# Optimization experiments

Hardware: AMD Instinct MI355X
Metric: run time of the kernel (lower is better)

## Reference

```python
import jax, jax.numpy as jnp
import numpy as np


def setup_inputs() -> dict:
    key = jax.random.key(0)
    ks = jax.random.split(key, 6)
    B, S, H, I, E = 2, 1024, 1024, 2816, 8
    W = 0.02  # weight init scale
    return {
        "x": jax.random.normal(ks[0], (B, S, H), jnp.float32),
        "w_router": jax.random.normal(ks[1], (H, E), jnp.float32) * W,
        "w_gate": jax.random.normal(ks[2], (E, H, I), jnp.float32) * W,
        "w_up": jax.random.normal(ks[3], (E, H, I), jnp.float32) * W,
        "w_down": jax.random.normal(ks[4], (E, I, H), jnp.float32) * W,
        "b_down": jnp.zeros((E, H), jnp.float32),
    }


def reference(x, w_router, w_gate, w_up, w_down, b_down):
    # Eval path of PrunedLlamaSMoEBlock: noiseless router, top-k select, softmax
    # over selected logits, SwiGLU experts, scatter-add combine.
    NUM_SELECTS = 2
    T = x.shape[0] * x.shape[1]
    E = w_router.shape[1]
    flat_x = x.reshape(T, -1)                      # [T,H]

    logits = flat_x @ w_router                     # [T,E]
    top_vals, top_idx = jax.lax.top_k(logits, NUM_SELECTS)   # [T,k]
    gw = jax.nn.softmax(top_vals.astype(jnp.float32), axis=1).astype(x.dtype)

    # Dense combine weights: combine[t,e] = sum_k gw[t,k] * (top_idx[t,k]==e)
    combine = jnp.zeros((T, E), x.dtype).at[
        jnp.arange(T)[:, None], top_idx
    ].add(gw)                                      # [T,E]

    # SwiGLU experts over all tokens (weighted by combine, zero if unselected)
    g = jnp.einsum("th,ehi->tei", flat_x, w_gate)  # [T,E,I]
    u = jnp.einsum("th,ehi->tei", flat_x, w_up)    # [T,E,I]
    a = jax.nn.silu(g) * u                         # [T,E,I]
    y = jnp.einsum("tei,eih->teh", a, w_down) + b_down[None]  # [T,E,H]

    out = jnp.einsum("te,teh->th", combine, y)     # [T,H]
    return out.reshape(x.shape)
```

## Files before the change

### kernel.cpp

```cpp
#include <hip/hip_runtime.h>
#include <math.h>

#define HD __device__ __forceinline__

constexpr int TT = 2048;
constexpr int HH = 1024;
constexpr int II = 2816;
constexpr int EE = 8;
constexpr int NK1 = HH / 64;
constexpr int NK2 = II / 64;
constexpr int KS2 = 2;
constexpr int HALF2 = NK2 / KS2;
constexpr int MAXTILES = 40;
constexpr int NSLOT = 2 * TT;

typedef short  bf16x8  __attribute__((ext_vector_type(8)));
typedef float  floatx4 __attribute__((ext_vector_type(4)));
typedef unsigned short ushortx8 __attribute__((ext_vector_type(8)));

constexpr size_t OFF_XB    = 0;
constexpr size_t OFF_WGT   = OFF_XB    + (size_t)TT*HH*2;
constexpr size_t OFF_WUT   = OFF_WGT   + (size_t)EE*II*HH*2;
constexpr size_t OFF_WDT   = OFF_WUT   + (size_t)EE*II*HH*2;
constexpr size_t OFF_ABUF  = OFF_WDT   + (size_t)EE*HH*II*2;
constexpr size_t OFF_CNT   = OFF_ABUF  + (size_t)2*TT*II*2;
constexpr size_t OFF_OFFS  = OFF_CNT   + 256;
constexpr size_t OFF_MDESC = OFF_OFFS  + 256;
constexpr size_t OFF_EMETA = OFF_MDESC + 256;
constexpr size_t OFF_WMETA = OFF_EMETA + 16384;
constexpr size_t OFF_TLIST = OFF_WMETA + 16384;
constexpr size_t OFF_SLOT  = OFF_TLIST + 16384;
constexpr size_t OFF_YBUF  = OFF_WGT;

HD unsigned short f2bf(float f) {
  union { float f; unsigned int u; } v; v.f = f;
  return (unsigned short)((v.u + 0x7fffu + ((v.u >> 16) & 1u)) >> 16);
}

HD void load_lds16(const void* gptr, void* lptr) {
  __builtin_amdgcn_global_load_lds(
      (const __attribute__((address_space(1))) void*)gptr,
      (__attribute__((address_space(3))) void*)lptr,
      16, 0, 0);
}

__global__ __launch_bounds__(256)
void prep_kernel(const float* __restrict__ x, unsigned short* __restrict__ xb,
                 int* __restrict__ counts) {
  const int i = blockIdx.x * blockDim.x + threadIdx.x;
  if (i < EE) counts[i] = 0;
  float4 v = ((const float4*)x)[i];
  ushort4 o;
  o.x = f2bf(v.x); o.y = f2bf(v.y); o.z = f2bf(v.z); o.w = f2bf(v.w);
  ((ushort4*)xb)[i] = o;
}

__global__ __launch_bounds__(256)
void transpose_cast_kernel(const float* __restrict__ wg, const float* __restrict__ wu,
                           const float* __restrict__ wd,
                           unsigned short* __restrict__ wgt, unsigned short* __restrict__ wut,
                           unsigned short* __restrict__ wdt) {
  const int e = blockIdx.y / 3;
  const int t = blockIdx.y % 3;
  const float* src; unsigned short* dst; int R, C;
  if (t == 0)      { src = wg; dst = wgt; R = HH; C = II; }
  else if (t == 1) { src = wu; dst = wut; R = HH; C = II; }
  else             { src = wd; dst = wdt; R = II; C = HH; }
  const int nct = C / 128;
  const int rt = blockIdx.x / nct;
  const int ct = blockIdx.x % nct;
  const size_t base = (size_t)e * R * C;
  const int R0 = rt * 64;
  const int C0 = ct * 128;

  const int lane = threadIdx.x & 63;
  const int wave = threadIdx.x >> 6;
  const int r0 = R0 + (lane & 7) * 8;
  const int c0 = C0 + wave * 32 + (lane >> 3) * 4;

  floatx4 v[8];
  const float* sp = src + base + (size_t)r0 * C + c0;
#pragma unroll
  for (int j = 0; j < 8; ++j)
    v[j] = __builtin_nontemporal_load((const floatx4*)(sp + (size_t)j * C));

  unsigned short* dp = dst + base + (size_t)c0 * R + r0;
#pragma unroll
  for (int jj = 0; jj < 4; ++jj) {
    ushortx8 o;
#pragma unroll
    for (int j = 0; j < 8; ++j) o[j] = f2bf(v[j][jj]);
    *(ushortx8*)(dp + (size_t)jj * R) = o;
  }
}

__global__ __launch_bounds__(64)
void router_kernel(const float* __restrict__ x, const float* __restrict__ w_router,
                   int* __restrict__ counts, int* __restrict__ emeta, float* __restrict__ wmeta) {
  const int t = blockIdx.x;
  const int lane = threadIdx.x;
  float acc[EE];
#pragma unroll
  for (int e = 0; e < EE; ++e) acc[e] = 0.f;
  for (int h = lane; h < HH; h += 64) {
    const float xv = x[(size_t)t * HH + h];
    const float* wr = w_router + (size_t)h * EE;
#pragma unroll
    for (int e = 0; e < EE; ++e) acc[e] += xv * wr[e];
  }
#pragma unroll
  for (int e = 0; e < EE; ++e) {
#pragma unroll
    for (int off = 32; off > 0; off >>= 1) acc[e] += __shfl_xor(acc[e], off, 64);
  }
  if (lane == 0) {
    int e0 = 0; float v0 = acc[0];
#pragma unroll
    for (int e = 1; e < EE; ++e) if (acc[e] > v0) { v0 = acc[e]; e0 = e; }
    int e1 = -1; float v1 = -3.4e38f;
#pragma unroll
    for (int e = 0; e < EE; ++e) if (e != e0 && acc[e] > v1) { v1 = acc[e]; e1 = e; }
    const float ex = __expf(v1 - v0);
    const float s  = 1.f + ex;
    emeta[2 * t] = e0; emeta[2 * t + 1] = e1;
    wmeta[2 * t] = 1.f / s; wmeta[2 * t + 1] = ex / s;
    atomicAdd(&counts[e0], 1);
    atomicAdd(&counts[e1], 1);
  }
}

__global__ __launch_bounds__(256)
void scanfill_kernel(const int* __restrict__ counts, const int* __restrict__ emeta,
                     int* __restrict__ offsets, int* __restrict__ mdesc,
                     int* __restrict__ token_list, int* __restrict__ slotmap) {
  const int e = blockIdx.x;
  const int tid = threadIdx.x;
  int off_e = 0;
#pragma unroll
  for (int i = 0; i < EE; ++i) { const int c = counts[i]; if (i < e) off_e += c; }
  if (e == 0 && tid == 0) {
    int s = 0, nt = 0;
    for (int i = 0; i < EE; ++i) {
      const int c = counts[i];
      offsets[i] = s;
      for (int m = 0; m < c; m += 128) mdesc[1 + nt++] = (i << 20) | m;
      s += c;
    }
    offsets[EE] = s;
    mdesc[0] = nt;
  }
  constexpr int CH = TT / 256;
  const int t0 = tid * CH;
  int cnt = 0;
  for (int k = 0; k < CH; ++k) {
    const int t = t0 + k;
    if (emeta[2 * t] == e) ++cnt;
    if (emeta[2 * t + 1] == e) ++cnt;
  }
  __shared__ int s_scan[256];
  s_scan[tid] = cnt;
  __syncthreads();
  int v = cnt;
  for (int d = 1; d < 256; d <<= 1) {
    const int add = (tid >= d) ? s_scan[tid - d] : 0;
    __syncthreads();
    v += add;
    s_scan[tid] = v;
    __syncthreads();
  }
  int pos = off_e + (v - cnt);
  for (int k = 0; k < CH; ++k) {
    const int t = t0 + k;
#pragma unroll
    for (int s = 0; s < 2; ++s) {
      if (emeta[2 * t + s] == e) {
        token_list[pos] = t;
        slotmap[2 * t + s] = pos;
        ++pos;
      }
    }
  }
}

__global__ __launch_bounds__(256, 4)
void gemm1_kernel(const unsigned short* __restrict__ xb,
                  const unsigned short* __restrict__ wgt,
                  const unsigned short* __restrict__ wut,
                  const int* __restrict__ offsets,
                  const int* __restrict__ mdesc,
                  const int* __restrict__ token_list,
                  unsigned short* __restrict__ Abuf) {
  if ((int)blockIdx.y >= mdesc[0]) return;
  const int d = mdesc[1 + blockIdx.y];
  const int e = d >> 20;
  const int m_base = d & 0xFFFFF;
  const int off_e = offsets[e];
  const int n_e = offsets[e + 1] - off_e;
  const int n_base = blockIdx.x * 64;

  __shared__ __attribute__((aligned(16))) unsigned short ldsA[128 * 64];
  __shared__ __attribute__((aligned(16))) unsigned short ldsG[64 * 64];
  __shared__ __attribute__((aligned(16))) unsigned short ldsU[64 * 64];

  const int tid = threadIdx.x;
  const int wave = tid >> 6;
  const int lane = tid & 63;
  const int quad = lane >> 4;
  const int l16 = lane & 15;
  const int wave_m = (wave & 1) * 64;
  const int wave_n = (wave >> 1) * 32;

  const int srow = lane >> 3;
  const int clog = (lane & 7) ^ srow;

  const unsigned short* gA[4];
  const unsigned short* gG[2];
  const unsigned short* gU[2];
#pragma unroll
  for (int it = 0; it < 4; ++it) {
    const int r = it * 32 + wave * 8 + srow;
    int ar = m_base + r; if (ar > n_e - 1) ar = n_e - 1;
    const int tok = token_list[off_e + ar];
    gA[it] = xb + (size_t)tok * HH + clog * 8;
  }
#pragma unroll
  for (int it = 0; it < 2; ++it) {
    const int r = it * 32 + wave * 8 + srow;
    gG[it] = wgt + ((size_t)e * II + (n_base + r)) * HH + clog * 8;
    gU[it] = wut + ((size_t)e * II + (n_base + r)) * HH + clog * 8;
  }

  floatx4 accG[4][2], accU[4][2];
  const floatx4 fz = {0.f, 0.f, 0.f, 0.f};
#pragma unroll
  for (int i = 0; i < 4; ++i)
#pragma unroll
    for (int j = 0; j < 2; ++j) { accG[i][j] = fz; accU[i][j] = fz; }

  for (int kt = 0; kt < NK1; ++kt) {
    const int k0 = kt * 64;
#pragma unroll
    for (int it = 0; it < 4; ++it)
      load_lds16(gA[it] + k0, &ldsA[(it * 32 + wave * 8) * 64]);
#pragma unroll
    for (int it = 0; it < 2; ++it) {
      load_lds16(gG[it] + k0, &ldsG[(it * 32 + wave * 8) * 64]);
      load_lds16(gU[it] + k0, &ldsU[(it * 32 + wave * 8) * 64]);
    }
    __syncthreads();
#pragma unroll
    for (int ks = 0; ks < 2; ++ks) {
      bf16x8 af[4], bg[2], bu[2];
#pragma unroll
      for (int f = 0; f < 4; ++f) {
        const int rowA = wave_m + f * 16 + l16;
        const int cA = (ks * 4 + quad) ^ (rowA & 7);
        af[f] = *(const bf16x8*)&ldsA[rowA * 64 + cA * 8];
      }
#pragma unroll
      for (int f = 0; f < 2; ++f) {
        const int rowB = wave_n + f * 16 + l16;
        const int cB = (ks * 4 + quad) ^ (rowB & 7);
        bg[f] = *(const bf16x8*)&ldsG[rowB * 64 + cB * 8];
        bu[f] = *(const bf16x8*)&ldsU[rowB * 64 + cB * 8];
      }
#pragma unroll
      for (int mf = 0; mf < 4; ++mf)
#pragma unroll
        for (int nf = 0; nf < 2; ++nf) {
          accG[mf][nf] = __builtin_amdgcn_mfma_f32_16x16x32_bf16(af[mf], bg[nf], accG[mf][nf], 0, 0, 0);
          accU[mf][nf] = __builtin_amdgcn_mfma_f32_16x16x32_bf16(af[mf], bu[nf], accU[mf][nf], 0, 0, 0);
        }
    }
    __syncthreads();
  }

#pragma unroll
  for (int mf = 0; mf < 4; ++mf)
#pragma unroll
    for (int nf = 0; nf < 2; ++nf) {
      const int col = n_base + wave_n + nf * 16 + l16;
#pragma unroll
      for (int j = 0; j < 4; ++j) {
        const int r = m_base + wave_m + mf * 16 + quad * 4 + j;
        if (r < n_e) {
          const float g = accG[mf][nf][j];
          const float u = accU[mf][nf][j];
          const float a = (g / (1.f + __expf(-g))) * u;
          Abuf[(size_t)(off_e + r) * II + col] = f2bf(a);
        }
      }
    }
}

__global__ __launch_bounds__(256, 3)
void gemm2_kernel(const unsigned short* __restrict__ Abuf,
                  const unsigned short* __restrict__ wdt,
                  const int* __restrict__ offsets,
                  const int* __restrict__ mdesc,
                  float* __restrict__ Ybuf) {
  if ((int)blockIdx.y >= mdesc[0]) return;
  const int d = mdesc[1 + blockIdx.y];
  const int e = d >> 20;
  const int m_base = d & 0xFFFFF;
  const int off_e = offsets[e];
  const int n_e = offsets[e + 1] - off_e;
  const int n_base = blockIdx.x * 128;
  const int split = blockIdx.z;
  const int kt_lo = split * HALF2;
  const int kt_hi = kt_lo + HALF2;

  __shared__ __attribute__((aligned(16))) unsigned short ldsA[128 * 64];
  __shared__ __attribute__((aligned(16))) unsigned short ldsB[128 * 64];

  const int tid = threadIdx.x;
  const int wave = tid >> 6;
  const int lane = tid & 63;
  const int quad = lane >> 4;
  const int l16 = lane & 15;
  const int wave_m = (wave & 1) * 64;
  const int wave_n = (wave >> 1) * 64;

  const int srow = lane >> 3;
  const int clog = (lane & 7) ^ srow;

  const unsigned short* gA[4];
  const unsigned short* gB[4];
#pragma unroll
  for (int it = 0; it < 4; ++it) {
    const int r = it * 32 + wave * 8 + srow;
    int ar = m_base + r; if (ar > n_e - 1) ar = n_e - 1;
    gA[it] = Abuf + (size_t)(off_e + ar) * II + clog * 8;
  }
#pragma unroll
  for (int it = 0; it < 4; ++it) {
    const int r = it * 32 + wave * 8 + srow;
    gB[it] = wdt + ((size_t)e * HH + (n_base + r)) * II + clog * 8;
  }

  floatx4 acc[4][4];
  const floatx4 fz = {0.f, 0.f, 0.f, 0.f};
#pragma unroll
  for (int i = 0; i < 4; ++i)
#pragma unroll
    for (int j = 0; j < 4; ++j) acc[i][j] = fz;

  for (int kt = kt_lo; kt < kt_hi; ++kt) {
    const int k0 = kt * 64;
#pragma unroll
    for (int it = 0; it < 4; ++it)
      load_lds16(gA[it] + k0, &ldsA[(it * 32 + wave * 8) * 64]);
#pragma unroll
    for (int it = 0; it < 4; ++it)
      load_lds16(gB[it] + k0, &ldsB[(it * 32 + wave * 8) * 64]);
    __syncthreads();
#pragma unroll
    for (int ks = 0; ks < 2; ++ks) {
      bf16x8 af[4], bf[4];
#pragma unroll
      for (int f = 0; f < 4; ++f) {
        const int rowA = wave_m + f * 16 + l16;
        const int cA = (ks * 4 + quad) ^ (rowA & 7);
        af[f] = *(const bf16x8*)&ldsA[rowA * 64 + cA * 8];
      }
#pragma unroll
      for (int f = 0; f < 4; ++f) {
        const int rowB = wave_n + f * 16 + l16;
        const int cB = (ks * 4 + quad) ^ (rowB & 7);
        bf[f] = *(const bf16x8*)&ldsB[rowB * 64 + cB * 8];
      }
#pragma unroll
      for (int mf = 0; mf < 4; ++mf)
#pragma unroll
        for (int nf = 0; nf < 4; ++nf)
          acc[mf][nf] = __builtin_amdgcn_mfma_f32_16x16x32_bf16(af[mf], bf[nf], acc[mf][nf], 0, 0, 0);
    }
    __syncthreads();
  }

  float* yb = Ybuf + (size_t)split * NSLOT * HH;
#pragma unroll
  for (int mf = 0; mf < 4; ++mf)
#pragma unroll
    for (int nf = 0; nf < 4; ++nf) {
      const int col = n_base + wave_n + nf * 16 + l16;
#pragma unroll
      for (int j = 0; j < 4; ++j) {
        const int r = m_base + wave_m + mf * 16 + quad * 4 + j;
        if (r < n_e)
          yb[(size_t)(off_e + r) * HH + col] = acc[mf][nf][j];
      }
    }
}

__global__ __launch_bounds__(256)
void combine_kernel(const float* __restrict__ Ybuf, const int* __restrict__ slotmap,
                    const int* __restrict__ emeta, const float* __restrict__ wmeta,
                    const float* __restrict__ b_down, float* __restrict__ out) {
  const int t = blockIdx.x;
  const int c = threadIdx.x;
  const int s0 = slotmap[2 * t], s1 = slotmap[2 * t + 1];
  const int e0 = emeta[2 * t], e1 = emeta[2 * t + 1];
  const float g0 = wmeta[2 * t], g1 = wmeta[2 * t + 1];
  const float4 y00 = ((const float4*)(Ybuf + (size_t)s0 * HH))[c];
  const float4 y01 = ((const float4*)(Ybuf + ((size_t)NSLOT + s0) * HH))[c];
  const float4 y10 = ((const float4*)(Ybuf + (size_t)s1 * HH))[c];
  const float4 y11 = ((const float4*)(Ybuf + ((size_t)NSLOT + s1) * HH))[c];
  const float4 b0 = ((const float4*)(b_down + (size_t)e0 * HH))[c];
  const float4 b1 = ((const float4*)(b_down + (size_t)e1 * HH))[c];
  float4 o;
  o.x = g0 * (y00.x + y01.x + b0.x) + g1 * (y10.x + y11.x + b1.x);
  o.y = g0 * (y00.y + y01.y + b0.y) + g1 * (y10.y + y11.y + b1.y);
  o.z = g0 * (y00.z + y01.z + b0.z) + g1 * (y10.z + y11.z + b1.z);
  o.w = g0 * (y00.w + y01.w + b0.w) + g1 * (y10.w + y11.w + b1.w);
  ((float4*)(out + (size_t)t * HH))[c] = o;
}

extern "C" void kernel_launch(void* const* d_in, const int* in_sizes, int n_in,
                              void* d_out, int out_size, void* d_ws, size_t ws_size,
                              hipStream_t stream) {
  const float* x        = (const float*)d_in[0];
  const float* w_router = (const float*)d_in[1];
  const float* w_gate   = (const float*)d_in[2];
  const float* w_up     = (const float*)d_in[3];
  const float* w_down   = (const float*)d_in[4];
  const float* b_down   = (const float*)d_in[5];
  float* out = (float*)d_out;

  char* ws = (char*)d_ws;
  unsigned short* xb   = (unsigned short*)(ws + OFF_XB);
  unsigned short* wgt  = (unsigned short*)(ws + OFF_WGT);
  unsigned short* wut  = (unsigned short*)(ws + OFF_WUT);
  unsigned short* wdt  = (unsigned short*)(ws + OFF_WDT);
  unsigned short* Abuf = (unsigned short*)(ws + OFF_ABUF);
  int*   counts  = (int*)(ws + OFF_CNT);
  int*   offsets = (int*)(ws + OFF_OFFS);
  int*   mdesc   = (int*)(ws + OFF_MDESC);
  int*   emeta   = (int*)(ws + OFF_EMETA);
  float* wmeta   = (float*)(ws + OFF_WMETA);
  int*   tlist   = (int*)(ws + OFF_TLIST);
  int*   slotmap = (int*)(ws + OFF_SLOT);
  float* Ybuf    = (float*)(ws + OFF_YBUF);

  prep_kernel<<<TT * HH / 4 / 256, 256, 0, stream>>>(x, xb, counts);
  router_kernel<<<TT, 64, 0, stream>>>(x, w_router, counts, emeta, wmeta);
  scanfill_kernel<<<EE, 256, 0, stream>>>(counts, emeta, offsets, mdesc, tlist, slotmap);
  transpose_cast_kernel<<<dim3(352, 3 * EE), 256, 0, stream>>>(
      w_gate, w_up, w_down, wgt, wut, wdt);
  gemm1_kernel<<<dim3(II / 64, MAXTILES), 256, 0, stream>>>(xb, wgt, wut, offsets, mdesc, tlist, Abuf);
  gemm2_kernel<<<dim3(HH / 128, MAXTILES, KS2), 256, 0, stream>>>(Abuf, wdt, offsets, mdesc, Ybuf);
  combine_kernel<<<TT, 256, 0, stream>>>(Ybuf, slotmap, emeta, wmeta, b_down, out);
}
```

Before: 431.8 us.

## Fuse prep with router and scan with transpose; remap GEMM blocks across XCDs

Merges the bf16 cast of x with the router logits and top-2 selection in one kernel, with one wave per token. The per-expert scan and fill now run as an extra row of blocks inside the weight transpose kernel, which drops the global atomic counts and two launches. Both GEMM kernels now remap their linear block id so that consecutive work groups are spread across the 8 XCDs in contiguous chunks, aiming for better L2 reuse of weights. The cost is a more complex block index mapping and the scan blocks sharing a grid with the bandwidth-bound transpose.

```diff
diff --git a/kernel.cpp b/kernel.cpp
--- a/kernel.cpp
+++ b/kernel.cpp
@@ -45,21 +45,133 @@
 }
 
 __global__ __launch_bounds__(256)
-void prep_kernel(const float* __restrict__ x, unsigned short* __restrict__ xb,
-                 int* __restrict__ counts) {
-  const int i = blockIdx.x * blockDim.x + threadIdx.x;
-  if (i < EE) counts[i] = 0;
-  float4 v = ((const float4*)x)[i];
-  ushort4 o;
-  o.x = f2bf(v.x); o.y = f2bf(v.y); o.z = f2bf(v.z); o.w = f2bf(v.w);
-  ((ushort4*)xb)[i] = o;
+void prep_router_kernel(const float* __restrict__ x, const float* __restrict__ w_router,
+                        unsigned short* __restrict__ xb,
+                        int* __restrict__ emeta, float* __restrict__ wmeta) {
+  const int wave = threadIdx.x >> 6;
+  const int lane = threadIdx.x & 63;
+  const int t = blockIdx.x * 4 + wave;
+  const float* xr = x + (size_t)t * HH;
+  unsigned short* xo = xb + (size_t)t * HH;
+
+  float acc[EE];
+#pragma unroll
+  for (int e = 0; e < EE; ++e) acc[e] = 0.f;
+
+#pragma unroll
+  for (int it = 0; it < 4; ++it) {
+    const int h0 = it * 256 + lane * 4;
+    const float4 v = *(const float4*)(xr + h0);
+    ushort4 o;
+    o.x = f2bf(v.x); o.y = f2bf(v.y); o.z = f2bf(v.z); o.w = f2bf(v.w);
+    *(ushort4*)(xo + h0) = o;
+    const float vv[4] = {v.x, v.y, v.z, v.w};
+#pragma unroll
+    for (int j = 0; j < 4; ++j) {
+      const float* wr = w_router + (size_t)(h0 + j) * EE;
+      const float4 w0 = ((const float4*)wr)[0];
+      const float4 w1 = ((const float4*)wr)[1];
+      acc[0] += vv[j] * w0.x; acc[1] += vv[j] * w0.y;
+      acc[2] += vv[j] * w0.z; acc[3] += vv[j] * w0.w;
+      acc[4] += vv[j] * w1.x; acc[5] += vv[j] * w1.y;
+      acc[6] += vv[j] * w1.z; acc[7] += vv[j] * w1.w;
+    }
+  }
+#pragma unroll
+  for (int e = 0; e < EE; ++e) {
+#pragma unroll
+    for (int off = 32; off > 0; off >>= 1) acc[e] += __shfl_xor(acc[e], off, 64);
+  }
+  if (lane == 0) {
+    int e0 = 0; float v0 = acc[0];
+#pragma unroll
+    for (int e = 1; e < EE; ++e) if (acc[e] > v0) { v0 = acc[e]; e0 = e; }
+    int e1 = -1; float v1 = -3.4e38f;
+#pragma unroll
+    for (int e = 0; e < EE; ++e) if (e != e0 && acc[e] > v1) { v1 = acc[e]; e1 = e; }
+    const float ex = __expf(v1 - v0);
+    const float s  = 1.f + ex;
+    emeta[2 * t] = e0; emeta[2 * t + 1] = e1;
+    wmeta[2 * t] = 1.f / s; wmeta[2 * t + 1] = ex / s;
+  }
 }
 
 __global__ __launch_bounds__(256)
-void transpose_cast_kernel(const float* __restrict__ wg, const float* __restrict__ wu,
+void transpose_scan_kernel(const float* __restrict__ wg, const float* __restrict__ wu,
                            const float* __restrict__ wd,
                            unsigned short* __restrict__ wgt, unsigned short* __restrict__ wut,
-                           unsigned short* __restrict__ wdt) {
+                           unsigned short* __restrict__ wdt,
+                           const int* __restrict__ emeta,
+                           int* __restrict__ offsets, int* __restrict__ mdesc,
+                           int* __restrict__ token_list, int* __restrict__ slotmap) {
+  __shared__ int s_tot[EE];
+  __shared__ int s_scan[256];
+
+  if ((int)blockIdx.y == 3 * EE) {
+    if ((int)blockIdx.x >= EE) return;
+    const int e = blockIdx.x;
+    const int tid = threadIdx.x;
+    constexpr int CH = TT / 256;
+    const int t0 = tid * CH;
+    int lc[EE];
+#pragma unroll
+    for (int i = 0; i < EE; ++i) lc[i] = 0;
+    int ep[CH][2];
+#pragma unroll
+    for (int k = 0; k < CH; ++k) {
+      const int a = emeta[2 * (t0 + k)];
+      const int b = emeta[2 * (t0 + k) + 1];
+      ep[k][0] = a; ep[k][1] = b;
+#pragma unroll
+      for (int i = 0; i < EE; ++i) lc[i] += (a == i) + (b == i);
+    }
+    if (tid < EE) s_tot[tid] = 0;
+    __syncthreads();
+#pragma unroll
+    for (int i = 0; i < EE; ++i) if (lc[i]) atomicAdd(&s_tot[i], lc[i]);
+    int cnt = 0;
+#pragma unroll
+    for (int i = 0; i < EE; ++i) if (i == e) cnt = lc[i];
+    s_scan[tid] = cnt;
+    __syncthreads();
+    int v = cnt;
+    for (int d = 1; d < 256; d <<= 1) {
+      const int add = (tid >= d) ? s_scan[tid - d] : 0;
+      __syncthreads();
+      v += add;
+      s_scan[tid] = v;
+      __syncthreads();
+    }
+    int off_e = 0;
+#pragma unroll
+    for (int i = 0; i < EE; ++i) off_e += (i < e) ? s_tot[i] : 0;
+    if (e == 0 && tid == 0) {
+      int s = 0, nt = 0;
+      for (int i = 0; i < EE; ++i) {
+        const int c = s_tot[i];
+        offsets[i] = s;
+        for (int m = 0; m < c; m += 128) mdesc[1 + nt++] = (i << 20) | m;
+        s += c;
+      }
+      offsets[EE] = s;
+      mdesc[0] = nt;
+    }
+    int pos = off_e + (v - cnt);
+#pragma unroll
+    for (int k = 0; k < CH; ++k) {
+      const int t = t0 + k;
+#pragma unroll
+      for (int s = 0; s < 2; ++s) {
+        if (ep[k][s] == e) {
+          token_list[pos] = t;
+          slotmap[2 * t + s] = pos;
+          ++pos;
+        }
+      }
+    }
+    return;
+  }
+
   const int e = blockIdx.y / 3;
   const int t = blockIdx.y % 3;
   const float* src; unsigned short* dst; int R, C;
@@ -94,94 +206,6 @@
   }
 }
 
-__global__ __launch_bounds__(64)
-void router_kernel(const float* __restrict__ x, const float* __restrict__ w_router,
-                   int* __restrict__ counts, int* __restrict__ emeta, float* __restrict__ wmeta) {
-  const int t = blockIdx.x;
-  const int lane = threadIdx.x;
-  float acc[EE];
-#pragma unroll
-  for (int e = 0; e < EE; ++e) acc[e] = 0.f;
-  for (int h = lane; h < HH; h += 64) {
-    const float xv = x[(size_t)t * HH + h];
-    const float* wr = w_router + (size_t)h * EE;
-#pragma unroll
-    for (int e = 0; e < EE; ++e) acc[e] += xv * wr[e];
-  }
-#pragma unroll
-  for (int e = 0; e < EE; ++e) {
-#pragma unroll
-    for (int off = 32; off > 0; off >>= 1) acc[e] += __shfl_xor(acc[e], off, 64);
-  }
-  if (lane == 0) {
-    int e0 = 0; float v0 = acc[0];
-#pragma unroll
-    for (int e = 1; e < EE; ++e) if (acc[e] > v0) { v0 = acc[e]; e0 = e; }
-    int e1 = -1; float v1 = -3.4e38f;
-#pragma unroll
-    for (int e = 0; e < EE; ++e) if (e != e0 && acc[e] > v1) { v1 = acc[e]; e1 = e; }
-    const float ex = __expf(v1 - v0);
-    const float s  = 1.f + ex;
-    emeta[2 * t] = e0; emeta[2 * t + 1] = e1;
-    wmeta[2 * t] = 1.f / s; wmeta[2 * t + 1] = ex / s;
-    atomicAdd(&counts[e0], 1);
-    atomicAdd(&counts[e1], 1);
-  }
-}
-
-__global__ __launch_bounds__(256)
-void scanfill_kernel(const int* __restrict__ counts, const int* __restrict__ emeta,
-                     int* __restrict__ offsets, int* __restrict__ mdesc,
-                     int* __restrict__ token_list, int* __restrict__ slotmap) {
-  const int e = blockIdx.x;
-  const int tid = threadIdx.x;
-  int off_e = 0;
-#pragma unroll
-  for (int i = 0; i < EE; ++i) { const int c = counts[i]; if (i < e) off_e += c; }
-  if (e == 0 && tid == 0) {
-    int s = 0, nt = 0;
-    for (int i = 0; i < EE; ++i) {
-      const int c = counts[i];
-      offsets[i] = s;
-      for (int m = 0; m < c; m += 128) mdesc[1 + nt++] = (i << 20) | m;
-      s += c;
-    }
-    offsets[EE] = s;
-    mdesc[0] = nt;
-  }
-  constexpr int CH = TT / 256;
-  const int t0 = tid * CH;
-  int cnt = 0;
-  for (int k = 0; k < CH; ++k) {
-    const int t = t0 + k;
-    if (emeta[2 * t] == e) ++cnt;
-    if (emeta[2 * t + 1] == e) ++cnt;
-  }
-  __shared__ int s_scan[256];
-  s_scan[tid] = cnt;
-  __syncthreads();
-  int v = cnt;
-  for (int d = 1; d < 256; d <<= 1) {
-    const int add = (tid >= d) ? s_scan[tid - d] : 0;
-    __syncthreads();
-    v += add;
-    s_scan[tid] = v;
-    __syncthreads();
-  }
-  int pos = off_e + (v - cnt);
-  for (int k = 0; k < CH; ++k) {
-    const int t = t0 + k;
-#pragma unroll
-    for (int s = 0; s < 2; ++s) {
-      if (emeta[2 * t + s] == e) {
-        token_list[pos] = t;
-        slotmap[2 * t + s] = pos;
-        ++pos;
-      }
-    }
-  }
-}
-
 __global__ __launch_bounds__(256, 4)
 void gemm1_kernel(const unsigned short* __restrict__ xb,
                   const unsigned short* __restrict__ wgt,
@@ -190,13 +214,20 @@
                   const int* __restrict__ mdesc,
                   const int* __restrict__ token_list,
                   unsigned short* __restrict__ Abuf) {
-  if ((int)blockIdx.y >= mdesc[0]) return;
-  const int d = mdesc[1 + blockIdx.y];
+  constexpr int NWG1 = (II / 64) * MAXTILES;
+  constexpr int CHUNK1 = NWG1 / 8;
+  const int p = (int)(blockIdx.y * gridDim.x + blockIdx.x);
+  const int idx = (p & 7) * CHUNK1 + (p >> 3);
+  const int bx = idx / MAXTILES;
+  const int by = idx % MAXTILES;
+
+  if (by >= mdesc[0]) return;
+  const int d = mdesc[1 + by];
   const int e = d >> 20;
   const int m_base = d & 0xFFFFF;
   const int off_e = offsets[e];
   const int n_e = offsets[e + 1] - off_e;
-  const int n_base = blockIdx.x * 64;
+  const int n_base = bx * 64;
 
   __shared__ __attribute__((aligned(16))) unsigned short ldsA[128 * 64];
   __shared__ __attribute__((aligned(16))) unsigned short ldsG[64 * 64];
@@ -299,14 +330,20 @@
                   const int* __restrict__ offsets,
                   const int* __restrict__ mdesc,
                   float* __restrict__ Ybuf) {
-  if ((int)blockIdx.y >= mdesc[0]) return;
-  const int d = mdesc[1 + blockIdx.y];
+  const int p = (int)(blockIdx.x + gridDim.x * (blockIdx.y + gridDim.y * blockIdx.z));
+  const int idx = (p & 7) * 80 + (p >> 3);
+  const int by = idx % MAXTILES;
+  const int g = idx / MAXTILES;
+  const int bx = g & 7;
+  const int split = g >> 3;
+
+  if (by >= mdesc[0]) return;
+  const int d = mdesc[1 + by];
   const int e = d >> 20;
   const int m_base = d & 0xFFFFF;
   const int off_e = offsets[e];
   const int n_e = offsets[e + 1] - off_e;
-  const int n_base = blockIdx.x * 128;
-  const int split = blockIdx.z;
+  const int n_base = bx * 128;
   const int kt_lo = split * HALF2;
   const int kt_hi = kt_lo + HALF2;
 
@@ -433,7 +470,6 @@
   unsigned short* wut  = (unsigned short*)(ws + OFF_WUT);
   unsigned short* wdt  = (unsigned short*)(ws + OFF_WDT);
   unsigned short* Abuf = (unsigned short*)(ws + OFF_ABUF);
-  int*   counts  = (int*)(ws + OFF_CNT);
   int*   offsets = (int*)(ws + OFF_OFFS);
   int*   mdesc   = (int*)(ws + OFF_MDESC);
   int*   emeta   = (int*)(ws + OFF_EMETA);
@@ -442,11 +478,9 @@
   int*   slotmap = (int*)(ws + OFF_SLOT);
   float* Ybuf    = (float*)(ws + OFF_YBUF);
 
-  prep_kernel<<<TT * HH / 4 / 256, 256, 0, stream>>>(x, xb, counts);
-  router_kernel<<<TT, 64, 0, stream>>>(x, w_router, counts, emeta, wmeta);
-  scanfill_kernel<<<EE, 256, 0, stream>>>(counts, emeta, offsets, mdesc, tlist, slotmap);
-  transpose_cast_kernel<<<dim3(352, 3 * EE), 256, 0, stream>>>(
-      w_gate, w_up, w_down, wgt, wut, wdt);
+  prep_router_kernel<<<TT / 4, 256, 0, stream>>>(x, w_router, xb, emeta, wmeta);
+  transpose_scan_kernel<<<dim3(352, 3 * EE + 1), 256, 0, stream>>>(
+      w_gate, w_up, w_down, wgt, wut, wdt, emeta, offsets, mdesc, tlist, slotmap);
   gemm1_kernel<<<dim3(II / 64, MAXTILES), 256, 0, stream>>>(xb, wgt, wut, offsets, mdesc, tlist, Abuf);
   gemm2_kernel<<<dim3(HH / 128, MAXTILES, KS2), 256, 0, stream>>>(Abuf, wdt, offsets, mdesc, Ybuf);
   combine_kernel<<<TT, 256, 0, stream>>>(Ybuf, slotmap, emeta, wmeta, b_down, out);
```

After: 376.3 us. 12.9% less time.
